# Optimization experiments

Hardware: AMD Instinct MI355X
Metric: run time of the kernel (lower is better)

## Reference

```python
import jax, jax.numpy as jnp
import numpy as np

N_NODES = 50000
N_EDGES = 1_600_000
IN_DIM = 256
HIDDEN = 256
OUT_DIM = 48
K = 10
ALPHA = 0.5


def _ppr_temp(K, alpha):
    # PPR init from GPR_prop: temp[k] = alpha*(1-alpha)^k, temp[K] = (1-alpha)^K
    t = alpha * (1 - alpha) ** np.arange(K + 1, dtype=np.float32)
    t[-1] = (1 - alpha) ** K
    return jnp.asarray(t, dtype=jnp.float32)


def setup_inputs() -> dict:
    key = jax.random.key(0)
    ks = jax.random.split(key, 7)
    x = jax.random.normal(ks[0], (N_NODES, IN_DIM), dtype=jnp.float32)
    edge_index = jax.random.randint(ks[1], (2, N_EDGES), 0, N_NODES, dtype=jnp.int64)
    # Linear layers (torch Linear: y = x @ W.T + b); store as [in, out]
    lim1 = 1.0 / np.sqrt(IN_DIM)
    W1 = jax.random.uniform(ks[2], (IN_DIM, HIDDEN), jnp.float32, -lim1, lim1)
    b1 = jax.random.uniform(ks[3], (HIDDEN,), jnp.float32, -lim1, lim1)
    lim2 = 1.0 / np.sqrt(HIDDEN)
    W2 = jax.random.uniform(ks[4], (HIDDEN, OUT_DIM), jnp.float32, -lim2, lim2)
    b2 = jax.random.uniform(ks[5], (OUT_DIM,), jnp.float32, -lim2, lim2)
    temp = _ppr_temp(K, ALPHA)
    return {"x": x, "edge_index": edge_index, "W1": W1, "b1": b1,
            "W2": W2, "b2": b2, "temp": temp}


def reference(x, edge_index, W1, b1, W2, b2, temp):
    N = x.shape[0]
    # MLP head (dropout in eval mode -> identity)
    h = jax.nn.relu(x @ W1 + b1)
    h = h @ W2 + b2  # [N, OUT_DIM]

    # GCN normalization with self-loops: norm_e = deg^-1/2[src] * deg^-1/2[dst]
    loops = jnp.arange(N, dtype=edge_index.dtype)
    src = jnp.concatenate([edge_index[0], loops])
    dst = jnp.concatenate([edge_index[1], loops])
    deg = jnp.zeros((N,), dtype=h.dtype).at[dst].add(1.0)
    dinv = jax.lax.rsqrt(jnp.maximum(deg, 1e-12))
    norm = (dinv[src] * dinv[dst])[:, None]  # [E+N, 1]

    # K-hop propagation with learned gamma mixing
    def step(carry, gamma):
        hk, hidden = carry
        msg = norm * hk[src]                              # gather + scale
        hk = jax.ops.segment_sum(msg, dst, num_segments=N)  # scatter-add
        return (hk, hidden + gamma * hk), None

    (_, hidden), _ = jax.lax.scan(step, (h, temp[0] * h), temp[1:])
    return jax.nn.log_softmax(hidden, axis=1)
```

## Files before the change

### kernel.cpp

```cpp
#include <hip/hip_runtime.h>
#include <hip/hip_fp16.h>
#include <math.h>

#define BSH    9
#define BNODES 512
#define NBMAX  128
#define CAP2   24576
#define ECHUNK 6144

typedef short bf16x8 __attribute__((ext_vector_type(8)));
typedef float f32x4 __attribute__((ext_vector_type(4)));

__device__ __forceinline__ unsigned f2b(float f) {
    union { float f; unsigned u; } x; x.f = f;
    return (x.u + 0x7fffu + ((x.u >> 16) & 1u)) >> 16;
}


__global__ __launch_bounds__(256) void k_zero(int* __restrict__ p, int n) {
    int i = blockIdx.x * 256 + threadIdx.x;
    if (i < n) p[i] = 0;
}


__global__ __launch_bounds__(256) void k_castx(const float4* __restrict__ x, uint4* __restrict__ xb, int n8) {
    int i = blockIdx.x * 256 + threadIdx.x;
    if (i >= n8) return;
    float4 f0 = x[2 * i], f1 = x[2 * i + 1];
    uint4 o;
    o.x = f2b(f0.x) | (f2b(f0.y) << 16);
    o.y = f2b(f0.z) | (f2b(f0.w) << 16);
    o.z = f2b(f1.x) | (f2b(f1.y) << 16);
    o.w = f2b(f1.z) | (f2b(f1.w) << 16);
    xb[i] = o;
}

__global__ __launch_bounds__(256) void k_castw(const float* __restrict__ W1, const float* __restrict__ W2,
                                               unsigned short* __restrict__ w1t, unsigned short* __restrict__ w2t) {
    int i = blockIdx.x * 256 + threadIdx.x;
    if (i < 65536) {
        int n = i >> 8, k = i & 255;
        w1t[i] = (unsigned short)f2b(W1[k * 256 + n]);
    } else if (i < 65536 + 12288) {
        int j = i - 65536;
        int n = j >> 8, k = j & 255;
        w2t[j] = (unsigned short)f2b(W2[k * 48 + n]);
    }
}


__global__ __launch_bounds__(256) void k_bin(const int* __restrict__ src, const int* __restrict__ dst,
                                             int* __restrict__ bktcnt, unsigned* __restrict__ stage,
                                             int E, int NB) {
    __shared__ unsigned ecache[ECHUNK];
    __shared__ int lcnt[NBMAX], lbase[NBMAX], lcur[NBMAX];
    const int t = threadIdx.x;
    for (int i = t; i < NBMAX; i += 256) { lcnt[i] = 0; lcur[i] = 0; }
    const int e0 = blockIdx.x * ECHUNK;
    const int m = min(ECHUNK, E - e0);
    __syncthreads();
    for (int i = t; i < m; i += 256) {
        int s = src[e0 + i], d = dst[e0 + i];
        ecache[i] = ((unsigned)d << 16) | (unsigned)s;
        atomicAdd(&lcnt[d >> BSH], 1);
    }
    __syncthreads();
    if (t < NB) lbase[t] = lcnt[t] ? atomicAdd(&bktcnt[t], lcnt[t]) : 0;
    __syncthreads();
    for (int i = t; i < m; i += 256) {
        unsigned p = ecache[i];
        int b = (int)(p >> (16 + BSH));
        int pos = lbase[b] + atomicAdd(&lcur[b], 1);
        if (pos < CAP2) stage[(size_t)b * CAP2 + pos] = p;
    }
}


__global__ __launch_bounds__(512) void k_cnt(const unsigned* __restrict__ stage,
                                             const int* __restrict__ bktcnt,
                                             int* __restrict__ cnt,
                                             float* __restrict__ dinv, float* __restrict__ dinv2,
                                             float* __restrict__ sdeg, int N) {
    __shared__ int dcnt[BNODES];
    const int b = blockIdx.x, t = threadIdx.x;
    dcnt[t] = 0;
    __syncthreads();
    const int m = min(bktcnt[b], CAP2);
    const unsigned* st = stage + (size_t)b * CAP2;
    for (int i = t; i < m; i += 512)
        atomicAdd(&dcnt[(st[i] >> 16) & (BNODES - 1)], 1);
    __syncthreads();
    int node = b * BNODES + t;
    if (node <= N) {
        int c = dcnt[t];
        cnt[node] = c;
        float d = (float)c + 1.0f;
        float r = rsqrtf(d);
        dinv[node] = r;
        dinv2[node] = r * r;
        sdeg[node] = d * r;
    }
}


__global__ __launch_bounds__(256) void k_scan1(const int* __restrict__ cnt, int* __restrict__ rowptr,
                                               int* __restrict__ blk, int NT) {
    __shared__ int s[256];
    int t = threadIdx.x, i = blockIdx.x * 256 + t;
    int v = (i < NT) ? ((cnt[i] + 31) & ~31) : 0;
    s[t] = v; __syncthreads();
#pragma unroll
    for (int off = 1; off < 256; off <<= 1) {
        int x = (t >= off) ? s[t - off] : 0; __syncthreads();
        s[t] += x; __syncthreads();
    }
    if (i < NT) rowptr[i] = s[t] - v;
    if (t == 255) blk[blockIdx.x] = s[255];
}

__global__ __launch_bounds__(256) void k_scan2(int* __restrict__ blk, int nb) {
    __shared__ int s[256];
    int t = threadIdx.x;
    int v = (t < nb) ? blk[t] : 0;
    s[t] = v; __syncthreads();
#pragma unroll
    for (int off = 1; off < 256; off <<= 1) {
        int x = (t >= off) ? s[t - off] : 0; __syncthreads();
        s[t] += x; __syncthreads();
    }
    if (t < nb) blk[t] = s[t] - v;
}

__global__ __launch_bounds__(256) void k_scan3(int* __restrict__ rowptr, const int* __restrict__ blk, int NT) {
    int i = blockIdx.x * 256 + threadIdx.x;
    if (i < NT) rowptr[i] += blk[blockIdx.x];
}


__global__ __launch_bounds__(512) void k_place(const unsigned* __restrict__ stage,
                                               const int* __restrict__ bktcnt,
                                               const int* __restrict__ rowptr,
                                               unsigned short* __restrict__ csr, int N) {
    __shared__ int lcur[BNODES];
    const int b = blockIdx.x, t = threadIdx.x;
    const int node = b * BNODES + t;
    lcur[t] = (node < N) ? rowptr[node] : 0;
    __syncthreads();
    const int m = min(bktcnt[b], CAP2);
    const unsigned* st = stage + (size_t)b * CAP2;
    for (int i = t; i < m; i += 512) {
        unsigned p = st[i];
        int dl = (int)((p >> 16) & (BNODES - 1));
        int pos = atomicAdd(&lcur[dl], 1);
        csr[pos] = (unsigned short)(p & 0xffffu);
    }
    __syncthreads();
    if (node < N) {
        int e1 = rowptr[node + 1];
        for (int i = lcur[t]; i < e1; ++i) csr[i] = (unsigned short)N;
    }
}


__global__ __launch_bounds__(256) void k_mgemm1(const unsigned short* __restrict__ xb,
                                                const unsigned short* __restrict__ w1t,
                                                const float* __restrict__ bias,
                                                unsigned short* __restrict__ h1b, int M) {
    __shared__ unsigned short sbuf[128 * 136];
    unsigned short* As = sbuf;
    unsigned short* Bs = sbuf + 128 * 40;
    const int t = threadIdx.x;
    const int bm = blockIdx.x * 128;
    const int bn = blockIdx.y * 128;
    const int w = t >> 6, lane = t & 63;
    const int q = lane >> 4, l16 = lane & 15;

    f32x4 acc[2][8] = {};
    const int ar0 = t >> 2;
    const int kc  = t & 3;
    const int swz_st = ((kc ^ (ar0 & 3)) * 8);
    int gr0 = bm + ar0;       if (gr0 >= M) gr0 = M - 1;
    int gr1 = bm + ar0 + 64;  if (gr1 >= M) gr1 = M - 1;
    const int swz_rd = (q ^ (l16 & 3)) * 8;

    for (int k0 = 0; k0 < 256; k0 += 32) {
        uint4 a0 = *(const uint4*)&xb[(size_t)gr0 * 256 + k0 + kc * 8];
        uint4 a1 = *(const uint4*)&xb[(size_t)gr1 * 256 + k0 + kc * 8];
        uint4 b0 = *(const uint4*)&w1t[(size_t)(bn + ar0) * 256 + k0 + kc * 8];
        uint4 b1 = *(const uint4*)&w1t[(size_t)(bn + ar0 + 64) * 256 + k0 + kc * 8];
        __syncthreads();
        *(uint4*)&As[ar0 * 40 + swz_st] = a0;
        *(uint4*)&As[(ar0 + 64) * 40 + swz_st] = a1;
        *(uint4*)&Bs[ar0 * 40 + swz_st] = b0;
        *(uint4*)&Bs[(ar0 + 64) * 40 + swz_st] = b1;
        __syncthreads();
        bf16x8 af0 = *(bf16x8*)&As[(w * 32 + l16) * 40 + swz_rd];
        bf16x8 af1 = *(bf16x8*)&As[(w * 32 + 16 + l16) * 40 + swz_rd];
#pragma unroll
        for (int j = 0; j < 8; ++j) {
            bf16x8 bf = *(bf16x8*)&Bs[(j * 16 + l16) * 40 + swz_rd];
            acc[0][j] = __builtin_amdgcn_mfma_f32_16x16x32_bf16(af0, bf, acc[0][j], 0, 0, 0);
            acc[1][j] = __builtin_amdgcn_mfma_f32_16x16x32_bf16(af1, bf, acc[1][j], 0, 0, 0);
        }
    }
    __syncthreads();
#pragma unroll
    for (int j = 0; j < 8; ++j) {
        int col = j * 16 + l16;
        float bb = bias[bn + col];
#pragma unroll
        for (int i = 0; i < 2; ++i) {
#pragma unroll
            for (int r = 0; r < 4; ++r) {
                float v = fmaxf(acc[i][j][r] + bb, 0.f);
                sbuf[(w * 32 + i * 16 + q * 4 + r) * 136 + col] = (unsigned short)f2b(v);
            }
        }
    }
    __syncthreads();
    const int row = t >> 1;
    const int ch = (t & 1) * 64;
    if (bm + row < M) {
#pragma unroll
        for (int i = 0; i < 8; ++i) {
            uint4 v = *(uint4*)&sbuf[row * 136 + ch + i * 8];
            *(uint4*)&h1b[(size_t)(bm + row) * 256 + bn + ch + i * 8] = v;
        }
    }
}


__global__ __launch_bounds__(256) void k_mgemm2(const unsigned short* __restrict__ h1b,
                                                const unsigned short* __restrict__ w2t,
                                                const float* __restrict__ bias,
                                                const float* __restrict__ dinv,
                                                __half* __restrict__ u0, int M) {
    __shared__ unsigned short As[128 * 40];
    __shared__ unsigned short Bs[48 * 40];
    const int t = threadIdx.x;
    const int bm = blockIdx.x * 128;
    const int w = t >> 6, lane = t & 63;
    const int q = lane >> 4, l16 = lane & 15;

    f32x4 acc[2][3] = {};
    const int ar0 = t >> 2;
    const int kc  = t & 3;
    const int swz_st = ((kc ^ (ar0 & 3)) * 8);
    int gr0 = bm + ar0;      if (gr0 >= M) gr0 = M - 1;
    int gr1 = bm + ar0 + 64; if (gr1 >= M) gr1 = M - 1;
    const int swz_rd = (q ^ (l16 & 3)) * 8;

    for (int k0 = 0; k0 < 256; k0 += 32) {
        uint4 a0 = *(const uint4*)&h1b[(size_t)gr0 * 256 + k0 + kc * 8];
        uint4 a1 = *(const uint4*)&h1b[(size_t)gr1 * 256 + k0 + kc * 8];
        uint4 bv;
        if (t < 192) bv = *(const uint4*)&w2t[(size_t)ar0 * 256 + k0 + kc * 8];
        __syncthreads();
        *(uint4*)&As[ar0 * 40 + swz_st] = a0;
        *(uint4*)&As[(ar0 + 64) * 40 + swz_st] = a1;
        if (t < 192) *(uint4*)&Bs[ar0 * 40 + swz_st] = bv;
        __syncthreads();
        bf16x8 af0 = *(bf16x8*)&As[(w * 32 + l16) * 40 + swz_rd];
        bf16x8 af1 = *(bf16x8*)&As[(w * 32 + 16 + l16) * 40 + swz_rd];
#pragma unroll
        for (int j = 0; j < 3; ++j) {
            bf16x8 bf = *(bf16x8*)&Bs[(j * 16 + l16) * 40 + swz_rd];
            acc[0][j] = __builtin_amdgcn_mfma_f32_16x16x32_bf16(af0, bf, acc[0][j], 0, 0, 0);
            acc[1][j] = __builtin_amdgcn_mfma_f32_16x16x32_bf16(af1, bf, acc[1][j], 0, 0, 0);
        }
    }
#pragma unroll
    for (int j = 0; j < 3; ++j) {
        int col = j * 16 + l16;
        float bb = bias[col];
#pragma unroll
        for (int i = 0; i < 2; ++i) {
#pragma unroll
            for (int r = 0; r < 4; ++r) {
                int row = bm + w * 32 + i * 16 + q * 4 + r;
                if (row < M) {
                    float v = (acc[i][j][r] + bb) * dinv[row];
                    u0[(size_t)row * 48 + col] = __float2half(v);
                }
            }
        }
    }
}


__global__ __launch_bounds__(256) void k_hop(const __half* __restrict__ u, __half* __restrict__ unxt,
                                             const int* __restrict__ rowptr,
                                             const unsigned short* __restrict__ csr,
                                             const float* __restrict__ dinv2, int NT) {
    int n = blockIdx.x * 4 + (threadIdx.x >> 6);
    if (n >= NT) return;
    const int lane = threadIdx.x & 63;
    const int j = lane & 7;
    const int cc = lane >> 3;
    const bool act = cc < 6;
    const int ccs = act ? cc : 0;

    float acc[8] = {0.f, 0.f, 0.f, 0.f, 0.f, 0.f, 0.f, 0.f};
    int e0 = rowptr[n], e1 = rowptr[n + 1];
    for (int e = e0; e < e1; e += 32) {
        int sa = (int)csr[e + j];
        int sb = (int)csr[e + 8 + j];
        int sc = (int)csr[e + 16 + j];
        int sd = (int)csr[e + 24 + j];
        union { uint4 u4; __half2 h2[4]; } ga, gb, gc, gd;
        ga.u4 = *(const uint4*)(u + (size_t)sa * 48 + ccs * 8);
        gb.u4 = *(const uint4*)(u + (size_t)sb * 48 + ccs * 8);
        gc.u4 = *(const uint4*)(u + (size_t)sc * 48 + ccs * 8);
        gd.u4 = *(const uint4*)(u + (size_t)sd * 48 + ccs * 8);
#pragma unroll
        for (int i = 0; i < 4; ++i) {
            float2 fa = __half22float2(ga.h2[i]);
            float2 fb = __half22float2(gb.h2[i]);
            float2 fc = __half22float2(gc.h2[i]);
            float2 fd = __half22float2(gd.h2[i]);
            acc[2 * i]     += (fa.x + fb.x) + (fc.x + fd.x);
            acc[2 * i + 1] += (fa.y + fb.y) + (fc.y + fd.y);
        }
    }
#pragma unroll
    for (int off = 1; off < 8; off <<= 1) {
#pragma unroll
        for (int i = 0; i < 8; ++i) acc[i] += __shfl_xor(acc[i], off);
    }
    if (act && j == 0) {
        union { uint4 u4; __half2 h2[4]; } sv, ov;
        sv.u4 = *(const uint4*)(u + (size_t)n * 48 + cc * 8);
        float w2 = dinv2[n];
#pragma unroll
        for (int i = 0; i < 4; ++i) {
            float2 sf = __half22float2(sv.h2[i]);
            float2 r;
            r.x = (acc[2 * i]     + sf.x) * w2;
            r.y = (acc[2 * i + 1] + sf.y) * w2;
            ov.h2[i] = __float22half2_rn(r);
        }
        *(uint4*)(unxt + (size_t)n * 48 + cc * 8) = ov.u4;
    }
}


__global__ __launch_bounds__(256) void k_final(const __half* __restrict__ u0, const __half* __restrict__ u1,
                                               size_t S, const float* __restrict__ sdeg,
                                               const float* __restrict__ temp,
                                               float* __restrict__ out, int N) {
    int w = (blockIdx.x * 256 + threadIdx.x) >> 6;
    int lane = threadIdx.x & 63;
    if (w >= N) return;
    size_t base = (size_t)w * 48 + lane;
    float val = 0.f, m = -INFINITY;
    if (lane < 48) {
        float acc = temp[0] * __half2float(u0[base]);
        const __half* uk = u1;
#pragma unroll
        for (int k = 1; k <= 10; ++k) {
            acc += temp[k] * __half2float(uk[base]);
            uk += S;
        }
        val = acc * sdeg[w];
        m = val;
    }
#pragma unroll
    for (int off = 32; off; off >>= 1) m = fmaxf(m, __shfl_xor(m, off));
    float ex = (lane < 48) ? __expf(val - m) : 0.f;
    float s = ex;
#pragma unroll
    for (int off = 32; off; off >>= 1) s += __shfl_xor(s, off);
    if (lane < 48) out[(size_t)w * 48 + lane] = val - m - __logf(s);
}


extern "C" void kernel_launch(void* const* d_in, const int* in_sizes, int n_in,
                              void* d_out, int out_size, void* d_ws, size_t ws_size,
                              hipStream_t stream) {
    const float* x    = (const float*)d_in[0];
    const int*   ei   = (const int*)d_in[1];
    const float* W1   = (const float*)d_in[2];
    const float* b1   = (const float*)d_in[3];
    const float* W2   = (const float*)d_in[4];
    const float* b2   = (const float*)d_in[5];
    const float* temp = (const float*)d_in[6];
    float* out = (float*)d_out;

    const int N = in_sizes[0] / 256;
    const int E = in_sizes[1] / 2;
    const int* src = ei;
    const int* dst = ei + E;

    const int NT  = N + 1;
    const int NT2 = N + 2;
    const int NB  = (NT + BNODES - 1) >> BSH;

    char* w8 = (char*)d_ws;
    size_t NP = (size_t)((NT2 + 63) & ~63);
    int*   cnt     = (int*)w8;
    int*   bktcnt  = cnt + NP;
    int*   rowptr  = bktcnt + 128;
    int*   blk     = rowptr + NP;
    float* dinv    = (float*)(blk + 256);
    float* dinv2   = dinv + NP;
    float* sdeg    = dinv2 + NP;
    unsigned short* csr = (unsigned short*)(sdeg + NP);
    size_t csr_i   = (((size_t)E + 32 * NT) / 2 + 32 + 63) & ~(size_t)63;
    unsigned short* w1t = (unsigned short*)((int*)(sdeg + NP) + csr_i);
    unsigned short* w2t = w1t + 65536;
    unsigned short* xb  = w2t + 12288 + 64;
    size_t S       = ((size_t)NT * 48 + 127) & ~(size_t)127;
    __half* u0     = (__half*)(xb + (size_t)N * 256);
    unsigned short* h1b = (unsigned short*)(u0 + S);
    unsigned* stage = (unsigned*)h1b;
    __half* u1     = (__half*)(h1b + (size_t)N * 256);

    const int nbS = (NT2 + 255) / 256;

    k_zero  <<<(int)((NP + 128 + 255) / 256), 256, 0, stream>>>(cnt, (int)(NP + 128));
    k_bin   <<<(E + ECHUNK - 1) / ECHUNK, 256, 0, stream>>>(src, dst, bktcnt, stage, E, NB);
    k_cnt   <<<NB, 512, 0, stream>>>(stage, bktcnt, cnt, dinv, dinv2, sdeg, N);
    k_scan1 <<<nbS, 256, 0, stream>>>(cnt, rowptr, blk, NT2);
    k_scan2 <<<1, 256, 0, stream>>>(blk, nbS);
    k_scan3 <<<nbS, 256, 0, stream>>>(rowptr, blk, NT2);
    k_place <<<NB, 512, 0, stream>>>(stage, bktcnt, rowptr, csr, N);

    k_castx <<<(N * 256 / 8 + 255) / 256, 256, 0, stream>>>((const float4*)x, (uint4*)xb, N * 256 / 8);
    k_castw <<<(65536 + 12288 + 255) / 256, 256, 0, stream>>>(W1, W2, w1t, w2t);

    dim3 g1((N + 127) / 128, 2);
    k_mgemm1<<<g1, 256, 0, stream>>>(xb, w1t, b1, h1b, N);
    k_mgemm2<<<(N + 127) / 128, 256, 0, stream>>>(h1b, w2t, b2, dinv, u0, N);
    k_zero  <<<1, 64, 0, stream>>>((int*)(u0 + (size_t)N * 48), 24);

    const int hopBlocks = (NT + 3) / 4;
    for (int k = 0; k < 10; ++k) {
        const __half* cur = (k == 0) ? u0 : (u1 + (size_t)(k - 1) * S);
        __half* nxt = u1 + (size_t)k * S;
        k_hop<<<hopBlocks, 256, 0, stream>>>(cur, nxt, rowptr, csr, dinv2, NT);
    }

    k_final<<<(N + 3) / 4, 256, 0, stream>>>(u0, u1, S, sdeg, temp, out, N);
}
```

Baseline: 506.9 us.

## Remove CSR row padding and remap hop lanes so every lane gathers

Rows in the CSR are no longer padded to multiples of 32 with dummy entries, so k_place stops writing pad entries and k_hop stops gathering a zero row. k_hop now maps all 64 lanes to work: lanes cover the first 32 halves of each row (16 edges at once) and the last 16 halves (32 edges at once), where before 16 of 64 lanes sat idle. A masked tail handles the leftover edges. The cost is a longer cross-lane shuffle reduction and a divergent remainder branch.

```diff
diff --git a/kernel.cpp b/kernel.cpp
--- a/kernel.cpp
+++ b/kernel.cpp
@@ -107,7 +107,7 @@
                                                int* __restrict__ blk, int NT) {
     __shared__ int s[256];
     int t = threadIdx.x, i = blockIdx.x * 256 + t;
-    int v = (i < NT) ? ((cnt[i] + 31) & ~31) : 0;
+    int v = (i < NT) ? cnt[i] : 0;
     s[t] = v; __syncthreads();
 #pragma unroll
     for (int off = 1; off < 256; off <<= 1) {
@@ -153,11 +153,6 @@
         int dl = (int)((p >> 16) & (BNODES - 1));
         int pos = atomicAdd(&lcur[dl], 1);
         csr[pos] = (unsigned short)(p & 0xffffu);
-    }
-    __syncthreads();
-    if (node < N) {
-        int e1 = rowptr[node + 1];
-        for (int i = lcur[t]; i < e1; ++i) csr[i] = (unsigned short)N;
     }
 }
 
@@ -295,51 +290,90 @@
     int n = blockIdx.x * 4 + (threadIdx.x >> 6);
     if (n >= NT) return;
     const int lane = threadIdx.x & 63;
-    const int j = lane & 7;
-    const int cc = lane >> 3;
-    const bool act = cc < 6;
-    const int ccs = act ? cc : 0;
-
-    float acc[8] = {0.f, 0.f, 0.f, 0.f, 0.f, 0.f, 0.f, 0.f};
-    int e0 = rowptr[n], e1 = rowptr[n + 1];
-    for (int e = e0; e < e1; e += 32) {
-        int sa = (int)csr[e + j];
-        int sb = (int)csr[e + 8 + j];
-        int sc = (int)csr[e + 16 + j];
-        int sd = (int)csr[e + 24 + j];
-        union { uint4 u4; __half2 h2[4]; } ga, gb, gc, gd;
-        ga.u4 = *(const uint4*)(u + (size_t)sa * 48 + ccs * 8);
-        gb.u4 = *(const uint4*)(u + (size_t)sb * 48 + ccs * 8);
-        gc.u4 = *(const uint4*)(u + (size_t)sc * 48 + ccs * 8);
-        gd.u4 = *(const uint4*)(u + (size_t)sd * 48 + ccs * 8);
+    const int cx = lane & 3;
+    const int jx = lane >> 2;
+    const int cy = lane & 1;
+    const int jy = lane >> 1;
+
+    float accX[8] = {0.f, 0.f, 0.f, 0.f, 0.f, 0.f, 0.f, 0.f};
+    float accY[8] = {0.f, 0.f, 0.f, 0.f, 0.f, 0.f, 0.f, 0.f};
+    const int e0 = rowptr[n], e1 = rowptr[n + 1];
+    int e = e0;
+    for (; e + 32 <= e1; e += 32) {
+        int sx0 = (int)csr[e + jx];
+        int sx1 = (int)csr[e + 16 + jx];
+        int sy  = (int)csr[e + jy];
+        union { uint4 u4; __half2 h2[4]; } gx0, gx1, gy;
+        gx0.u4 = *(const uint4*)(u + (size_t)sx0 * 48 + cx * 8);
+        gx1.u4 = *(const uint4*)(u + (size_t)sx1 * 48 + cx * 8);
+        gy.u4  = *(const uint4*)(u + (size_t)sy  * 48 + 32 + cy * 8);
 #pragma unroll
         for (int i = 0; i < 4; ++i) {
-            float2 fa = __half22float2(ga.h2[i]);
-            float2 fb = __half22float2(gb.h2[i]);
-            float2 fc = __half22float2(gc.h2[i]);
-            float2 fd = __half22float2(gd.h2[i]);
-            acc[2 * i]     += (fa.x + fb.x) + (fc.x + fd.x);
-            acc[2 * i + 1] += (fa.y + fb.y) + (fc.y + fd.y);
-        }
-    }
-#pragma unroll
-    for (int off = 1; off < 8; off <<= 1) {
-#pragma unroll
-        for (int i = 0; i < 8; ++i) acc[i] += __shfl_xor(acc[i], off);
-    }
-    if (act && j == 0) {
+            float2 f0 = __half22float2(gx0.h2[i]);
+            float2 f1 = __half22float2(gx1.h2[i]);
+            float2 fy = __half22float2(gy.h2[i]);
+            accX[2 * i]     += f0.x + f1.x;
+            accX[2 * i + 1] += f0.y + f1.y;
+            accY[2 * i]     += fy.x;
+            accY[2 * i + 1] += fy.y;
+        }
+    }
+    if (e < e1) {
+        const int rem = e1 - e;
+        union { uint4 u4; __half2 h2[4]; } gx0, gx1, gy;
+        gx0.u4 = make_uint4(0u, 0u, 0u, 0u);
+        gx1.u4 = make_uint4(0u, 0u, 0u, 0u);
+        gy.u4  = make_uint4(0u, 0u, 0u, 0u);
+        if (jx < rem)      gx0.u4 = *(const uint4*)(u + (size_t)((int)csr[e + jx]) * 48 + cx * 8);
+        if (16 + jx < rem) gx1.u4 = *(const uint4*)(u + (size_t)((int)csr[e + 16 + jx]) * 48 + cx * 8);
+        if (jy < rem)      gy.u4  = *(const uint4*)(u + (size_t)((int)csr[e + jy]) * 48 + 32 + cy * 8);
+#pragma unroll
+        for (int i = 0; i < 4; ++i) {
+            float2 f0 = __half22float2(gx0.h2[i]);
+            float2 f1 = __half22float2(gx1.h2[i]);
+            float2 fy = __half22float2(gy.h2[i]);
+            accX[2 * i]     += f0.x + f1.x;
+            accX[2 * i + 1] += f0.y + f1.y;
+            accY[2 * i]     += fy.x;
+            accY[2 * i + 1] += fy.y;
+        }
+    }
+#pragma unroll
+    for (int off = 4; off < 64; off <<= 1) {
+#pragma unroll
+        for (int i = 0; i < 8; ++i) accX[i] += __shfl_xor(accX[i], off);
+    }
+#pragma unroll
+    for (int off = 2; off < 64; off <<= 1) {
+#pragma unroll
+        for (int i = 0; i < 8; ++i) accY[i] += __shfl_xor(accY[i], off);
+    }
+    if (lane < 6) {
+        float a0 = (lane < 4) ? accX[0] : accY[0];
+        float a1 = (lane < 4) ? accX[1] : accY[1];
+        float a2 = (lane < 4) ? accX[2] : accY[2];
+        float a3 = (lane < 4) ? accX[3] : accY[3];
+        float a4 = (lane < 4) ? accX[4] : accY[4];
+        float a5 = (lane < 4) ? accX[5] : accY[5];
+        float a6 = (lane < 4) ? accX[6] : accY[6];
+        float a7 = (lane < 4) ? accX[7] : accY[7];
         union { uint4 u4; __half2 h2[4]; } sv, ov;
-        sv.u4 = *(const uint4*)(u + (size_t)n * 48 + cc * 8);
+        sv.u4 = *(const uint4*)(u + (size_t)n * 48 + lane * 8);
         float w2 = dinv2[n];
-#pragma unroll
-        for (int i = 0; i < 4; ++i) {
-            float2 sf = __half22float2(sv.h2[i]);
-            float2 r;
-            r.x = (acc[2 * i]     + sf.x) * w2;
-            r.y = (acc[2 * i + 1] + sf.y) * w2;
-            ov.h2[i] = __float22half2_rn(r);
-        }
-        *(uint4*)(unxt + (size_t)n * 48 + cc * 8) = ov.u4;
+        float2 sf0 = __half22float2(sv.h2[0]);
+        float2 sf1 = __half22float2(sv.h2[1]);
+        float2 sf2 = __half22float2(sv.h2[2]);
+        float2 sf3 = __half22float2(sv.h2[3]);
+        float2 r0, r1, r2, r3;
+        r0.x = (a0 + sf0.x) * w2;  r0.y = (a1 + sf0.y) * w2;
+        r1.x = (a2 + sf1.x) * w2;  r1.y = (a3 + sf1.y) * w2;
+        r2.x = (a4 + sf2.x) * w2;  r2.y = (a5 + sf2.y) * w2;
+        r3.x = (a6 + sf3.x) * w2;  r3.y = (a7 + sf3.y) * w2;
+        ov.h2[0] = __float22half2_rn(r0);
+        ov.h2[1] = __float22half2_rn(r1);
+        ov.h2[2] = __float22half2_rn(r2);
+        ov.h2[3] = __float22half2_rn(r3);
+        *(uint4*)(unxt + (size_t)n * 48 + lane * 8) = ov.u4;
     }
 }
 
```

After: 635.9 us. 1.25x slower.
